# Performance work log

Hardware: AMD Instinct MI355X
Metric: run time of the kernel (lower is better)

Reference implementation:

```python
import jax, jax.numpy as jnp
import numpy as np

N = 131072   # number of profile points
S = 64       # n_samples (PSF samples per point)
D = H = W = 256


def setup_inputs() -> dict:
    key = jax.random.key(0)
    k1, k2, k3, k4, k5, k6 = jax.random.split(key, 6)
    x = jax.random.normal(k1, (1, 1, D, H, W), dtype=jnp.float32)
    # voxel-space coordinates (x, y, z) inside the volume
    sampleGrid = jax.random.uniform(k2, (N, 3), dtype=jnp.float32) * jnp.array(
        [W - 1, H - 1, D - 1], dtype=jnp.float32)
    # small axis-angle rotations + translations: [N, 1, 6]
    rot = jax.random.normal(k3, (N, 1, 3), dtype=jnp.float32) * 0.02
    trn = jax.random.normal(k4, (N, 1, 3), dtype=jnp.float32) * 2.0
    ax = jnp.concatenate([rot, trn], axis=-1)
    half = jax.random.uniform(k5, (N, 1, 3), minval=1.0, maxval=3.0, dtype=jnp.float32)
    bound = jnp.concatenate([-half, half], axis=1)  # [N, 2, 3]
    InvCovScaled = jnp.eye(3, dtype=jnp.float32) * 0.5
    # torch.randn(...) - 0.5 from the original forward, hoisted out for determinism
    xyz_psf = jax.random.normal(k6, (N, S, 3), dtype=jnp.float32) - 0.5
    return dict(x=x, sampleGrid=sampleGrid, ax=ax, bound=bound,
                InvCovScaled=InvCovScaled, xyz_psf=xyz_psf)


def _axisangle2mat(a):
    # a: [N, 6] -> [N, 3, 4] = [R | t] via Rodrigues
    v, t = a[:, :3], a[:, 3:]
    theta = jnp.linalg.norm(v, axis=-1, keepdims=True)          # [N,1]
    k = v / jnp.maximum(theta, 1e-12)                            # unit axis
    kx, ky, kz = k[:, 0], k[:, 1], k[:, 2]
    z = jnp.zeros_like(kx)
    K = jnp.stack([z, -kz, ky, kz, z, -kx, -ky, kx, z], axis=-1).reshape(-1, 3, 3)
    ct = jnp.cos(theta)[..., None]  # [N,1,1]
    st = jnp.sin(theta)[..., None]
    I = jnp.eye(3, dtype=a.dtype)
    R = I + st * K + (1.0 - ct) * jnp.matmul(K, K)
    return jnp.concatenate([R, t[..., None]], axis=-1)           # [N,3,4]


def _grid_sample_3d(vol, grid):
    # vol: [D,H,W]; grid: [M,3] normalized coords (x,y,z) in [-1,1]
    # matches F.grid_sample(mode='bilinear', padding_mode='zeros', align_corners=False)
    d, h, w = vol.shape
    sizes = jnp.array([w, h, d], dtype=vol.dtype)
    pix = ((grid + 1.0) * sizes - 1.0) * 0.5                     # unnormalize
    ix, iy, iz = pix[:, 0], pix[:, 1], pix[:, 2]
    x0 = jnp.floor(ix); y0 = jnp.floor(iy); z0 = jnp.floor(iz)
    fx = ix - x0; fy = iy - y0; fz = iz - z0
    x0 = x0.astype(jnp.int32); y0 = y0.astype(jnp.int32); z0 = z0.astype(jnp.int32)

    def gather(xi, yi, zi):
        valid = ((xi >= 0) & (xi < w) & (yi >= 0) & (yi < h) & (zi >= 0) & (zi < d))
        xc = jnp.clip(xi, 0, w - 1)
        yc = jnp.clip(yi, 0, h - 1)
        zc = jnp.clip(zi, 0, d - 1)
        return jnp.where(valid, vol[zc, yc, xc], jnp.zeros((), vol.dtype))

    out = jnp.zeros(grid.shape[0], dtype=vol.dtype)
    for dx in (0, 1):
        wx = fx if dx else (1.0 - fx)
        for dy in (0, 1):
            wy = fy if dy else (1.0 - fy)
            for dz in (0, 1):
                wz = fz if dz else (1.0 - fz)
                out = out + gather(x0 + dx, y0 + dy, z0 + dz) * (wx * wy * wz)
    return out


def reference(x, sampleGrid, ax, bound, InvCovScaled, xyz_psf):
    vol = x[0, 0]                                                # [D,H,W]
    size = jnp.array([x.shape[-1], x.shape[-2], x.shape[-3]], dtype=x.dtype)  # [W,H,D]

    # pose matrices [N,1,3,4]
    mat = _axisangle2mat(ax.reshape(-1, 6)).reshape(ax.shape[:-1] + (3, 4))
    R = mat[..., :3]                                             # [N,1,3,3]
    T = mat[..., 3]                                              # [N,1,3]
    # trans_first=True: p' = R @ (p + T)
    p = sampleGrid[:, None] + T                                  # [N,1,3]
    mat_sampleGrid = jnp.einsum('nkij,nkj->nki', R, p)           # [N,1,3]

    # PSF offsets: [N,S,3]
    bound_psf = xyz_psf * ((bound[:, 1, :] - bound[:, 0, :]) * 0.5)[:, None]
    psf = mat_sampleGrid + bound_psf                             # [N,S,3]

    grid = 2.0 * (psf / (size - 1.0) - 0.5)                      # normalize per-axis
    psf_x = _grid_sample_3d(vol, grid.reshape(-1, 3)).reshape(psf.shape[:-1])  # [N,S]

    center = bound_psf
    q = jnp.einsum('nsi,ij,nsj->ns', center, InvCovScaled, center)
    w = jnp.exp(-0.5 * q)                                        # [N,S]
    y = (psf_x * w).sum(-1) / w.sum(-1)                          # [N]
    return y
```

## Files before the change

kernel.cpp:

```cpp
#include <hip/hip_runtime.h>


#define VOL_N 256
#define S_PSF 64
#define NBUCKET 4096
#define PAIRS_ELEMS (1 << 24)
#define PAIRS_BYTES ((size_t)PAIRS_ELEMS * 8)

typedef float vf4 __attribute__((ext_vector_type(4)));


__device__ __forceinline__ int bucket_of(const float* __restrict__ sg, int n) {
    int cx = min(max((int)sg[n * 3 + 0], 0), VOL_N - 1) >> 4;
    int cy = min(max((int)sg[n * 3 + 1], 0), VOL_N - 1) >> 4;
    int cz = min(max((int)sg[n * 3 + 2], 0), VOL_N - 1) >> 4;
    int m = 0;
    #pragma unroll
    for (int b = 0; b < 4; b++) {
        m |= (((cx >> b) & 1) << (3 * b))
           | (((cy >> b) & 1) << (3 * b + 1))
           | (((cz >> b) & 1) << (3 * b + 2));
    }
    return m;
}

__global__ void zero_hist_kernel(int* __restrict__ ws) {
    int i = blockIdx.x * blockDim.x + threadIdx.x;
    if (i < NBUCKET) ws[i] = 0;
}

__global__ void hist_kernel(const float* __restrict__ sg, int* __restrict__ ws, int N) {
    int n = blockIdx.x * blockDim.x + threadIdx.x;
    if (n >= N) return;
    atomicAdd(&ws[bucket_of(sg, n)], 1);
}

__global__ __launch_bounds__(1024) void scan_kernel(int* __restrict__ ws) {
    __shared__ int tmp[1024];
    const int t = threadIdx.x;
    int h0 = ws[t * 4 + 0], h1 = ws[t * 4 + 1], h2 = ws[t * 4 + 2], h3 = ws[t * 4 + 3];
    int s = h0 + h1 + h2 + h3;
    tmp[t] = s;
    __syncthreads();
    for (int off = 1; off < 1024; off <<= 1) {
        int v = (t >= off) ? tmp[t - off] : 0;
        __syncthreads();
        tmp[t] += v;
        __syncthreads();
    }
    int excl = tmp[t] - s;
    ws[NBUCKET + t * 4 + 0] = excl;
    ws[NBUCKET + t * 4 + 1] = excl + h0;
    ws[NBUCKET + t * 4 + 2] = excl + h0 + h1;
    ws[NBUCKET + t * 4 + 3] = excl + h0 + h1 + h2;
}

__global__ void scatter_kernel(const float* __restrict__ sg, int* __restrict__ ws, int N) {
    int n = blockIdx.x * blockDim.x + threadIdx.x;
    if (n >= N) return;
    int b = bucket_of(sg, n);
    int pos = atomicAdd(&ws[NBUCKET + b], 1);
    ws[2 * NBUCKET + pos] = n;
}

__global__ __launch_bounds__(256) void build_pairs_kernel(
    const float* __restrict__ vol, float* __restrict__ pairs) {
    const int g4 = blockIdx.x * blockDim.x + threadIdx.x;
    const int g = g4 << 2;
    const vf4 v = *(const vf4*)(vol + g);
    const int x = g & (VOL_N - 1);
    const float nxt = (x == VOL_N - 4) ? v.w : __builtin_nontemporal_load(vol + g + 4);
    vf4* dst = (vf4*)(pairs + (size_t)g * 2);
    vf4 a; a.x = v.x; a.y = v.y; a.z = v.y; a.w = v.z;
    vf4 b; b.x = v.z; b.y = v.w; b.z = v.w; b.w = nxt;
    __builtin_nontemporal_store(a, dst);
    __builtin_nontemporal_store(b, dst + 1);
}

template <bool USE_PAIRS>
__global__ __launch_bounds__(256, 4) void psf_sample_kernel(
    const float* __restrict__ vol,
    const float2* __restrict__ pairs,
    const float* __restrict__ sampleGrid,
    const float* __restrict__ ax,
    const float* __restrict__ bound,
    const float* __restrict__ invcov,
    const float* __restrict__ xyz_psf,
    const int* __restrict__ perm,
    float* __restrict__ out,
    int N)
{
    const int lane = threadIdx.x & 63;

    int bid = blockIdx.x;
    const int nb = gridDim.x;
    if ((nb & 7) == 0) bid = (bid & 7) * (nb >> 3) + (bid >> 3);

    const int i = bid * (blockDim.x >> 6) + (threadIdx.x >> 6);
    if (i >= N) return;
    const int n = perm ? perm[i] : i;

    const float vx = ax[n * 6 + 0], vy = ax[n * 6 + 1], vz = ax[n * 6 + 2];
    const float tx = ax[n * 6 + 3], ty = ax[n * 6 + 4], tz = ax[n * 6 + 5];

    const float theta = sqrtf(vx * vx + vy * vy + vz * vz);
    const float kinv = 1.0f / fmaxf(theta, 1e-12f);
    const float kx = vx * kinv, ky = vy * kinv, kz = vz * kinv;
    const float ct = __cosf(theta), st = __sinf(theta);
    const float oc = 1.0f - ct;

    const float r00 = 1.0f + oc * (-(ky * ky + kz * kz));
    const float r01 = -st * kz + oc * kx * ky;
    const float r02 =  st * ky + oc * kx * kz;
    const float r10 =  st * kz + oc * kx * ky;
    const float r11 = 1.0f + oc * (-(kx * kx + kz * kz));
    const float r12 = -st * kx + oc * ky * kz;
    const float r20 = -st * ky + oc * kx * kz;
    const float r21 =  st * kx + oc * ky * kz;
    const float r22 = 1.0f + oc * (-(kx * kx + ky * ky));

    const float px = sampleGrid[n * 3 + 0] + tx;
    const float py = sampleGrid[n * 3 + 1] + ty;
    const float pz = sampleGrid[n * 3 + 2] + tz;

    const float cx = r00 * px + r01 * py + r02 * pz;
    const float cy = r10 * px + r11 * py + r12 * pz;
    const float cz = r20 * px + r21 * py + r22 * pz;

    const float hx = (bound[n * 6 + 3] - bound[n * 6 + 0]) * 0.5f;
    const float hy = (bound[n * 6 + 4] - bound[n * 6 + 1]) * 0.5f;
    const float hz = (bound[n * 6 + 5] - bound[n * 6 + 2]) * 0.5f;

    const float m00 = invcov[0], m01 = invcov[1], m02 = invcov[2];
    const float m10 = invcov[3], m11 = invcov[4], m12 = invcov[5];
    const float m20 = invcov[6], m21 = invcov[7], m22 = invcov[8];

    const long long base = ((long long)n * S_PSF + lane) * 3;
    const float ox = xyz_psf[base + 0] * hx;
    const float oy = xyz_psf[base + 1] * hy;
    const float oz = xyz_psf[base + 2] * hz;

    const float scale = (float)VOL_N / (float)(VOL_N - 1);
    const float ix = (cx + ox) * scale - 0.5f;
    const float iy = (cy + oy) * scale - 0.5f;
    const float iz = (cz + oz) * scale - 0.5f;

    const float x0f = floorf(ix), y0f = floorf(iy), z0f = floorf(iz);
    const float fx = ix - x0f, fy = iy - y0f, fz = iz - z0f;
    const int x0 = (int)x0f, y0 = (int)y0f, z0 = (int)z0f;
    const int x1 = x0 + 1, y1 = y0 + 1, z1 = z0 + 1;

    const bool vx0 = (unsigned)x0 < (unsigned)VOL_N;
    const bool vx1 = (unsigned)x1 < (unsigned)VOL_N;
    const bool vy0 = (unsigned)y0 < (unsigned)VOL_N;
    const bool vy1 = (unsigned)y1 < (unsigned)VOL_N;
    const bool vz0 = (unsigned)z0 < (unsigned)VOL_N;
    const bool vz1 = (unsigned)z1 < (unsigned)VOL_N;

    const int yc0 = min(max(y0, 0), VOL_N - 1);
    const int yc1 = min(max(y1, 0), VOL_N - 1);
    const int zc0 = min(max(z0, 0), VOL_N - 1);
    const int zc1 = min(max(z1, 0), VOL_N - 1);
    const int zo0 = zc0 << 16, zo1 = zc1 << 16;
    const int yo0 = yc0 << 8, yo1 = yc1 << 8;

    float v000, v001, v010, v011, v100, v101, v110, v111;
    if (USE_PAIRS) {
        const int xg = min(max(x0, 0), VOL_N - 2);
        const int dx = x0 - xg;
        const bool hi = (dx == 1), lo = (dx == -1);
        const float2 p00 = pairs[zo0 + yo0 + xg];
        const float2 p01 = pairs[zo0 + yo1 + xg];
        const float2 p10 = pairs[zo1 + yo0 + xg];
        const float2 p11 = pairs[zo1 + yo1 + xg];
        v000 = hi ? p00.y : p00.x;  v001 = lo ? p00.x : p00.y;
        v010 = hi ? p01.y : p01.x;  v011 = lo ? p01.x : p01.y;
        v100 = hi ? p10.y : p10.x;  v101 = lo ? p10.x : p10.y;
        v110 = hi ? p11.y : p11.x;  v111 = lo ? p11.x : p11.y;
    } else {
        const int xc0 = min(max(x0, 0), VOL_N - 1);
        const int xc1 = min(max(x1, 0), VOL_N - 1);
        v000 = vol[zo0 + yo0 + xc0];
        v001 = vol[zo0 + yo0 + xc1];
        v010 = vol[zo0 + yo1 + xc0];
        v011 = vol[zo0 + yo1 + xc1];
        v100 = vol[zo1 + yo0 + xc0];
        v101 = vol[zo1 + yo0 + xc1];
        v110 = vol[zo1 + yo1 + xc0];
        v111 = vol[zo1 + yo1 + xc1];
    }

    const float wx0 = 1.0f - fx, wx1 = fx;
    const float wy0 = 1.0f - fy, wy1 = fy;
    const float wz0 = 1.0f - fz, wz1 = fz;

    float acc = 0.0f;
    acc += (vx0 && vy0 && vz0) ? v000 * (wx0 * wy0 * wz0) : 0.0f;
    acc += (vx1 && vy0 && vz0) ? v001 * (wx1 * wy0 * wz0) : 0.0f;
    acc += (vx0 && vy1 && vz0) ? v010 * (wx0 * wy1 * wz0) : 0.0f;
    acc += (vx1 && vy1 && vz0) ? v011 * (wx1 * wy1 * wz0) : 0.0f;
    acc += (vx0 && vy0 && vz1) ? v100 * (wx0 * wy0 * wz1) : 0.0f;
    acc += (vx1 && vy0 && vz1) ? v101 * (wx1 * wy0 * wz1) : 0.0f;
    acc += (vx0 && vy1 && vz1) ? v110 * (wx0 * wy1 * wz1) : 0.0f;
    acc += (vx1 && vy1 && vz1) ? v111 * (wx1 * wy1 * wz1) : 0.0f;

    const float qx = m00 * ox + m01 * oy + m02 * oz;
    const float qy = m10 * ox + m11 * oy + m12 * oz;
    const float qz = m20 * ox + m21 * oy + m22 * oz;
    const float q = ox * qx + oy * qy + oz * qz;
    const float w = __expf(-0.5f * q);

    float num = acc * w;
    float den = w;
    #pragma unroll
    for (int m = 32; m >= 1; m >>= 1) {
        num += __shfl_xor(num, m, 64);
        den += __shfl_xor(den, m, 64);
    }
    if (lane == 0) out[n] = num / den;
}

extern "C" void kernel_launch(void* const* d_in, const int* in_sizes, int n_in,
                              void* d_out, int out_size, void* d_ws, size_t ws_size,
                              hipStream_t stream) {
    const float* x        = (const float*)d_in[0];
    const float* sg       = (const float*)d_in[1];
    const float* ax       = (const float*)d_in[2];
    const float* bound    = (const float*)d_in[3];
    const float* invcov   = (const float*)d_in[4];
    const float* xyz_psf  = (const float*)d_in[5];
    float* out            = (float*)d_out;

    const int N = in_sizes[1] / 3;
    const size_t sort_bytes = (size_t)(2 * NBUCKET + N) * sizeof(int);

    const bool use_pairs = ws_size >= PAIRS_BYTES + sort_bytes;
    const bool use_sort  = use_pairs || ws_size >= sort_bytes;

    float* pairs = use_pairs ? (float*)d_ws : nullptr;
    int* sort_ws = use_pairs ? (int*)((char*)d_ws + PAIRS_BYTES) : (int*)d_ws;

    int* perm = nullptr;
    if (use_sort) {
        zero_hist_kernel<<<(NBUCKET + 255) / 256, 256, 0, stream>>>(sort_ws);
        hist_kernel<<<(N + 255) / 256, 256, 0, stream>>>(sg, sort_ws, N);
        scan_kernel<<<1, 1024, 0, stream>>>(sort_ws);
        scatter_kernel<<<(N + 255) / 256, 256, 0, stream>>>(sg, sort_ws, N);
        perm = sort_ws + 2 * NBUCKET;
    }
    if (use_pairs) {
        build_pairs_kernel<<<(PAIRS_ELEMS / 4) / 256, 256, 0, stream>>>(x, pairs);
    }

    dim3 block(256);
    dim3 grid((N + 3) / 4);
    if (use_pairs) {
        psf_sample_kernel<true><<<grid, block, 0, stream>>>(
            x, (const float2*)pairs, sg, ax, bound, invcov, xyz_psf, perm, out, N);
    } else {
        psf_sample_kernel<false><<<grid, block, 0, stream>>>(
            x, nullptr, sg, ax, bound, invcov, xyz_psf, perm, out, N);
    }
}
```

Baseline: 375.8 us.

## Replace float pair table with fp16 2x2 quad table for trilinear gathers

Precomputes a per-voxel fp16 table holding the 2x2 (x,y) neighbourhood, so each trilinear sample needs two 8-byte gathers instead of four. The table stays the same size, but the sampler's gather count is halved. Volume values are stored in half precision, which adds rounding error relative to the fp32 reference. It also makes the point index wave-uniform via readfirstlane and narrows index arithmetic to 32-bit.

```diff
diff --git a/kernel.cpp b/kernel.cpp
--- a/kernel.cpp
+++ b/kernel.cpp
@@ -4,10 +4,12 @@
 #define VOL_N 256
 #define S_PSF 64
 #define NBUCKET 4096
-#define PAIRS_ELEMS (1 << 24)
-#define PAIRS_BYTES ((size_t)PAIRS_ELEMS * 8)
+#define TBL_ELEMS (1 << 24)
+#define TBL_BYTES ((size_t)TBL_ELEMS * 8)
 
 typedef float vf4 __attribute__((ext_vector_type(4)));
+typedef _Float16 vh4 __attribute__((ext_vector_type(4)));
+typedef _Float16 vh8 __attribute__((ext_vector_type(8)));
 
 
 __device__ __forceinline__ int bucket_of(const float* __restrict__ sg, int n) {
@@ -63,24 +65,33 @@
     ws[2 * NBUCKET + pos] = n;
 }
 
-__global__ __launch_bounds__(256) void build_pairs_kernel(
-    const float* __restrict__ vol, float* __restrict__ pairs) {
-    const int g4 = blockIdx.x * blockDim.x + threadIdx.x;
-    const int g = g4 << 2;
-    const vf4 v = *(const vf4*)(vol + g);
-    const int x = g & (VOL_N - 1);
-    const float nxt = (x == VOL_N - 4) ? v.w : __builtin_nontemporal_load(vol + g + 4);
-    vf4* dst = (vf4*)(pairs + (size_t)g * 2);
-    vf4 a; a.x = v.x; a.y = v.y; a.z = v.y; a.w = v.z;
-    vf4 b; b.x = v.z; b.y = v.w; b.z = v.w; b.w = nxt;
-    __builtin_nontemporal_store(a, dst);
-    __builtin_nontemporal_store(b, dst + 1);
-}
-
-template <bool USE_PAIRS>
+__global__ __launch_bounds__(256) void build_quad_kernel(
+    const float* __restrict__ vol, vh4* __restrict__ tbl) {
+    const int t = blockIdx.x * 256 + threadIdx.x;
+    const int x4 = (t & 63) << 2;
+    const int y = (t >> 6) & 255;
+    const int z = t >> 14;
+    const float* r0 = vol + (z << 16) + (y << 8);
+    const float* r1 = vol + (z << 16) + (min(y + 1, VOL_N - 1) << 8);
+    const vf4 a = *(const vf4*)(r0 + x4);
+    const vf4 b = *(const vf4*)(r1 + x4);
+    const float a4 = (x4 == VOL_N - 4) ? a.w : r0[x4 + 4];
+    const float b4 = (x4 == VOL_N - 4) ? b.w : r1[x4 + 4];
+
+    union { vh8 h; vf4 f; } o0, o1;
+    o0.h = (vh8){(_Float16)a.x, (_Float16)a.y, (_Float16)b.x, (_Float16)b.y,
+                 (_Float16)a.y, (_Float16)a.z, (_Float16)b.y, (_Float16)b.z};
+    o1.h = (vh8){(_Float16)a.z, (_Float16)a.w, (_Float16)b.z, (_Float16)b.w,
+                 (_Float16)a.w, (_Float16)a4,  (_Float16)b.w, (_Float16)b4};
+    vf4* dst = (vf4*)(tbl + ((z << 16) + (y << 8) + x4));
+    __builtin_nontemporal_store(o0.f, dst);
+    __builtin_nontemporal_store(o1.f, dst + 1);
+}
+
+template <bool USE_TBL>
 __global__ __launch_bounds__(256, 4) void psf_sample_kernel(
     const float* __restrict__ vol,
-    const float2* __restrict__ pairs,
+    const vh4* __restrict__ tbl,
     const float* __restrict__ sampleGrid,
     const float* __restrict__ ax,
     const float* __restrict__ bound,
@@ -98,7 +109,7 @@
 
     const int i = bid * (blockDim.x >> 6) + (threadIdx.x >> 6);
     if (i >= N) return;
-    const int n = perm ? perm[i] : i;
+    const int n = __builtin_amdgcn_readfirstlane(perm ? perm[i] : i);
 
     const float vx = ax[n * 6 + 0], vy = ax[n * 6 + 1], vz = ax[n * 6 + 2];
     const float tx = ax[n * 6 + 3], ty = ax[n * 6 + 4], tz = ax[n * 6 + 5];
@@ -135,10 +146,10 @@
     const float m10 = invcov[3], m11 = invcov[4], m12 = invcov[5];
     const float m20 = invcov[6], m21 = invcov[7], m22 = invcov[8];
 
-    const long long base = ((long long)n * S_PSF + lane) * 3;
-    const float ox = xyz_psf[base + 0] * hx;
-    const float oy = xyz_psf[base + 1] * hy;
-    const float oz = xyz_psf[base + 2] * hz;
+    const int pbase = (n * S_PSF + lane) * 3;
+    const float ox = xyz_psf[pbase + 0] * hx;
+    const float oy = xyz_psf[pbase + 1] * hy;
+    const float oz = xyz_psf[pbase + 2] * hz;
 
     const float scale = (float)VOL_N / (float)(VOL_N - 1);
     const float ix = (cx + ox) * scale - 0.5f;
@@ -157,29 +168,38 @@
     const bool vz0 = (unsigned)z0 < (unsigned)VOL_N;
     const bool vz1 = (unsigned)z1 < (unsigned)VOL_N;
 
-    const int yc0 = min(max(y0, 0), VOL_N - 1);
-    const int yc1 = min(max(y1, 0), VOL_N - 1);
-    const int zc0 = min(max(z0, 0), VOL_N - 1);
-    const int zc1 = min(max(z1, 0), VOL_N - 1);
-    const int zo0 = zc0 << 16, zo1 = zc1 << 16;
-    const int yo0 = yc0 << 8, yo1 = yc1 << 8;
+    const float wx0 = 1.0f - fx, wx1 = fx;
+    const float wy0 = 1.0f - fy, wy1 = fy;
+    const float wz0 = 1.0f - fz, wz1 = fz;
 
     float v000, v001, v010, v011, v100, v101, v110, v111;
-    if (USE_PAIRS) {
-        const int xg = min(max(x0, 0), VOL_N - 2);
-        const int dx = x0 - xg;
-        const bool hi = (dx == 1), lo = (dx == -1);
-        const float2 p00 = pairs[zo0 + yo0 + xg];
-        const float2 p01 = pairs[zo0 + yo1 + xg];
-        const float2 p10 = pairs[zo1 + yo0 + xg];
-        const float2 p11 = pairs[zo1 + yo1 + xg];
-        v000 = hi ? p00.y : p00.x;  v001 = lo ? p00.x : p00.y;
-        v010 = hi ? p01.y : p01.x;  v011 = lo ? p01.x : p01.y;
-        v100 = hi ? p10.y : p10.x;  v101 = lo ? p10.x : p10.y;
-        v110 = hi ? p11.y : p11.x;  v111 = lo ? p11.x : p11.y;
+    if (USE_TBL) {
+        const int xg = min(max(x0, 0), VOL_N - 1);
+        const int yg = min(max(y0, 0), VOL_N - 1);
+        const int zg0 = min(max(z0, 0), VOL_N - 1);
+        const int zg1 = min(max(z1, 0), VOL_N - 1);
+        const int common = (yg << 8) + xg;
+        const vh4 p0 = tbl[(zg0 << 16) + common];
+        const vh4 p1 = tbl[(zg1 << 16) + common];
+        const bool lox = x0 < 0;
+        const bool loy = y0 < 0;
+        float s00 = p0.x, s01 = p0.y, s10 = p0.z, s11 = p0.w;
+        float a01 = lox ? s00 : s01, a11 = lox ? s10 : s11;
+        v000 = s00;                 v001 = a01;
+        v010 = loy ? s00 : s10;     v011 = loy ? a01 : a11;
+        s00 = p1.x; s01 = p1.y; s10 = p1.z; s11 = p1.w;
+        a01 = lox ? s00 : s01; a11 = lox ? s10 : s11;
+        v100 = s00;                 v101 = a01;
+        v110 = loy ? s00 : s10;     v111 = loy ? a01 : a11;
     } else {
         const int xc0 = min(max(x0, 0), VOL_N - 1);
         const int xc1 = min(max(x1, 0), VOL_N - 1);
+        const int yc0 = min(max(y0, 0), VOL_N - 1);
+        const int yc1 = min(max(y1, 0), VOL_N - 1);
+        const int zc0 = min(max(z0, 0), VOL_N - 1);
+        const int zc1 = min(max(z1, 0), VOL_N - 1);
+        const int zo0 = zc0 << 16, zo1 = zc1 << 16;
+        const int yo0 = yc0 << 8, yo1 = yc1 << 8;
         v000 = vol[zo0 + yo0 + xc0];
         v001 = vol[zo0 + yo0 + xc1];
         v010 = vol[zo0 + yo1 + xc0];
@@ -189,10 +209,6 @@
         v110 = vol[zo1 + yo1 + xc0];
         v111 = vol[zo1 + yo1 + xc1];
     }
-
-    const float wx0 = 1.0f - fx, wx1 = fx;
-    const float wy0 = 1.0f - fy, wy1 = fy;
-    const float wz0 = 1.0f - fz, wz1 = fz;
 
     float acc = 0.0f;
     acc += (vx0 && vy0 && vz0) ? v000 * (wx0 * wy0 * wz0) : 0.0f;
@@ -234,11 +250,11 @@
     const int N = in_sizes[1] / 3;
     const size_t sort_bytes = (size_t)(2 * NBUCKET + N) * sizeof(int);
 
-    const bool use_pairs = ws_size >= PAIRS_BYTES + sort_bytes;
-    const bool use_sort  = use_pairs || ws_size >= sort_bytes;
-
-    float* pairs = use_pairs ? (float*)d_ws : nullptr;
-    int* sort_ws = use_pairs ? (int*)((char*)d_ws + PAIRS_BYTES) : (int*)d_ws;
+    const bool use_tbl  = ws_size >= TBL_BYTES + sort_bytes;
+    const bool use_sort = use_tbl || ws_size >= sort_bytes;
+
+    vh4* tbl = use_tbl ? (vh4*)d_ws : nullptr;
+    int* sort_ws = use_tbl ? (int*)((char*)d_ws + TBL_BYTES) : (int*)d_ws;
 
     int* perm = nullptr;
     if (use_sort) {
@@ -248,15 +264,15 @@
         scatter_kernel<<<(N + 255) / 256, 256, 0, stream>>>(sg, sort_ws, N);
         perm = sort_ws + 2 * NBUCKET;
     }
-    if (use_pairs) {
-        build_pairs_kernel<<<(PAIRS_ELEMS / 4) / 256, 256, 0, stream>>>(x, pairs);
+    if (use_tbl) {
+        build_quad_kernel<<<(VOL_N * VOL_N * VOL_N / 4) / 256, 256, 0, stream>>>(x, tbl);
     }
 
     dim3 block(256);
     dim3 grid((N + 3) / 4);
-    if (use_pairs) {
+    if (use_tbl) {
         psf_sample_kernel<true><<<grid, block, 0, stream>>>(
-            x, (const float2*)pairs, sg, ax, bound, invcov, xyz_psf, perm, out, N);
+            x, tbl, sg, ax, bound, invcov, xyz_psf, perm, out, N);
     } else {
         psf_sample_kernel<false><<<grid, block, 0, stream>>>(
             x, nullptr, sg, ax, bound, invcov, xyz_psf, perm, out, N);
```

Result: faster. 329.3 us (-12.4%).
